# Kernel optimization log

Hardware: AMD Instinct MI355X
Metric: run time of the kernel (lower is better)

## Reference

```python
import jax, jax.numpy as jnp
import numpy as np

N_NODES = 100000
N_EDGES = 1600000
IN_C, HID_C, OUT_C = 64, 64, 16


def _sage_conv(x, src, dst, W_l, b_l, W_r, num_nodes):
    # PyG SAGEConv (aggr='mean'): out = lin_l(mean_{j->i} x_j) + lin_r(x_i)
    # aggregate first (cheap small-d features), then one GEMM
    msg_sum = jax.ops.segment_sum(x[src], dst, num_segments=num_nodes)
    deg = jax.ops.segment_sum(jnp.ones_like(dst, dtype=x.dtype), dst,
                              num_segments=num_nodes)
    mean = msg_sum / jnp.maximum(deg, 1.0)[:, None]
    return mean @ W_l + b_l + x @ W_r


def setup_inputs() -> dict:
    key = jax.random.key(0)
    ks = jax.random.split(key, 8)
    x = jax.random.normal(ks[0], (N_NODES, IN_C), dtype=jnp.float32)
    edge_index = jax.random.randint(ks[1], (2, N_EDGES), 0, N_NODES, dtype=jnp.int64)
    # Glorot-ish init for weights; lin_l has bias, lin_r has none (PyG default)
    def glorot(k, fan_in, fan_out):
        s = jnp.sqrt(6.0 / (fan_in + fan_out))
        return jax.random.uniform(k, (fan_in, fan_out), jnp.float32, -s, s)
    return {
        "x": x,
        "edge_index": edge_index,
        "W1_l": glorot(ks[2], IN_C, HID_C),
        "b1": jnp.zeros((HID_C,), jnp.float32),
        "W1_r": glorot(ks[3], IN_C, HID_C),
        "W2_l": glorot(ks[4], HID_C, OUT_C),
        "b2": jnp.zeros((OUT_C,), jnp.float32),
        "W2_r": glorot(ks[5], HID_C, OUT_C),
    }


def reference(x, edge_index, W1_l, b1, W1_r, W2_l, b2, W2_r):
    src, dst = edge_index[0], edge_index[1]
    h = _sage_conv(x, src, dst, W1_l, b1, W1_r, N_NODES)
    h = jax.nn.relu(h)
    # dropout p=0.3 is identity in eval mode
    out = _sage_conv(h, src, dst, W2_l, b2, W2_r, N_NODES)
    return out
```

## Files before the change

### kernel.cpp

```cpp
#include <hip/hip_runtime.h>
#include <hip/hip_fp16.h>

#define N_NODES 100000
#define N_EDGES 1600000
#define IN_C 64
#define HID_C 64
#define OUT_C 16

#define BKT 128
#define BSH 7
#define NBKT 782
#define CAP 2816
#define GSTR 32
#define GB 512
#define EPB 3125
#define NIT 13
#define G1B 1563

typedef _Float16 f16x8 __attribute__((ext_vector_type(8)));
typedef float f32x4 __attribute__((ext_vector_type(4)));
typedef float f32x16 __attribute__((ext_vector_type(16)));

__global__ __launch_bounds__(256) void k_merged1(
    const int* __restrict__ src, const int* __restrict__ dst,
    int* __restrict__ gcnt, int* __restrict__ binned,
    const float* __restrict__ x, const float* __restrict__ Wl,
    const float* __restrict__ Wr, const float* __restrict__ b,
    __half* __restrict__ p, __half* __restrict__ q) {
  __shared__ _Float16 sA[64 * 68];
  __shared__ _Float16 sW[128 * 68];
  int t = threadIdx.x;

  if (blockIdx.x < GB) {
    int* h   = (int*)sA;
    int* cur = (int*)sW;
    for (int i = t; i < NBKT; i += 256) h[i] = 0;
    __syncthreads();
    int base = blockIdx.x * EPB;
    int end = base + EPB;
    int dv[NIT], sv[NIT];
#pragma unroll
    for (int it = 0; it < NIT; ++it) {
      int e = base + t + it * 256;
      bool ok = (e < end);
      dv[it] = ok ? dst[e] : -1;
      sv[it] = ok ? src[e] : 0;
    }
#pragma unroll
    for (int it = 0; it < NIT; ++it)
      if (dv[it] >= 0) atomicAdd(&h[dv[it] >> BSH], 1);
    __syncthreads();
    for (int i = t; i < NBKT; i += 256) {
      int c = h[i];
      int b0 = (c > 0) ? atomicAdd(&gcnt[i * GSTR], c) : 0;
      cur[i] = i * CAP + b0;
    }
    __syncthreads();
#pragma unroll
    for (int it = 0; it < NIT; ++it) {
      if (dv[it] >= 0) {
        int d = dv[it];
        int pos = atomicAdd(&cur[d >> BSH], 1);
        binned[pos] = (sv[it] << BSH) | (d & (BKT - 1));
      }
    }
    return;
  }

  int n0 = (blockIdx.x - GB) * 64;

  for (int f = t; f < 1024; f += 256) {
    int r = f >> 4, c4 = f & 15;
    int n = n0 + r;
    float4 v = {0.0f, 0.0f, 0.0f, 0.0f};
    if (n < N_NODES) v = *(const float4*)&x[(size_t)n * 64 + c4 * 4];
    union { _Float16 h[4]; float2 f2; } u;
    u.h[0] = (_Float16)v.x; u.h[1] = (_Float16)v.y;
    u.h[2] = (_Float16)v.z; u.h[3] = (_Float16)v.w;
    *(float2*)&sA[r * 68 + c4 * 4] = u.f2;
  }
  for (int f = t; f < 2048; f += 256) {
    int k = f >> 5, c4 = f & 31;
    float4 w = (c4 < 16) ? *(const float4*)&Wl[k * 64 + c4 * 4]
                         : *(const float4*)&Wr[k * 64 + (c4 - 16) * 4];
    int c = c4 * 4;
    sW[(c + 0) * 68 + k] = (_Float16)w.x;
    sW[(c + 1) * 68 + k] = (_Float16)w.y;
    sW[(c + 2) * 68 + k] = (_Float16)w.z;
    sW[(c + 3) * 68 + k] = (_Float16)w.w;
  }
  __syncthreads();

  int w = t >> 6, lane = t & 63;
  int m = lane & 31, half = lane >> 5;
  int rt = w & 1, cg = w >> 1;

  f32x16 acc[2];
#pragma unroll
  for (int r = 0; r < 16; ++r) { acc[0][r] = 0.0f; acc[1][r] = 0.0f; }

  const _Float16* pA = &sA[(rt * 32 + m) * 68 + half * 8];
  const _Float16* pB0 = &sW[(cg * 64 + m) * 68 + half * 8];
  const _Float16* pB1 = &sW[(cg * 64 + 32 + m) * 68 + half * 8];
#pragma unroll
  for (int kc = 0; kc < 4; ++kc) {
    union { f16x8 v; float2 f2[2]; } a, b0, b1;
    a.f2[0] = *(const float2*)(pA + kc * 16);
    a.f2[1] = *(const float2*)(pA + kc * 16 + 4);
    b0.f2[0] = *(const float2*)(pB0 + kc * 16);
    b0.f2[1] = *(const float2*)(pB0 + kc * 16 + 4);
    b1.f2[0] = *(const float2*)(pB1 + kc * 16);
    b1.f2[1] = *(const float2*)(pB1 + kc * 16 + 4);
    acc[0] = __builtin_amdgcn_mfma_f32_32x32x16_f16(a.v, b0.v, acc[0], 0, 0, 0);
    acc[1] = __builtin_amdgcn_mfma_f32_32x32x16_f16(a.v, b1.v, acc[1], 0, 0, 0);
  }

  if (cg == 0) {
#pragma unroll
    for (int tt = 0; tt < 2; ++tt) {
      int col = tt * 32 + m;
#pragma unroll
      for (int r = 0; r < 16; ++r) {
        int row = (r & 3) + 4 * half + 8 * (r >> 2);
        int n = n0 + rt * 32 + row;
        if (n < N_NODES) p[(size_t)n * 64 + col] = __float2half(acc[tt][r]);
      }
    }
  } else {
    float bias[2] = {b[m], b[32 + m]};
#pragma unroll
    for (int tt = 0; tt < 2; ++tt) {
      int col = tt * 32 + m;
#pragma unroll
      for (int r = 0; r < 16; ++r) {
        int row = (r & 3) + 4 * half + 8 * (r >> 2);
        int n = n0 + rt * 32 + row;
        if (n < N_NODES)
          q[(size_t)n * 64 + col] = __float2half(acc[tt][r] + bias[tt]);
      }
    }
  }
}

__global__ __launch_bounds__(512) void k_fuse1c(
    const float4* __restrict__ p1, const int* __restrict__ gcnt,
    const int* __restrict__ binned, const float* __restrict__ W2l,
    const float* __restrict__ W2r, const float* __restrict__ b2,
    const float4* __restrict__ q1, int* __restrict__ csr,
    int* __restrict__ rowstart, int* __restrict__ cnt,
    __half* __restrict__ p2, float* __restrict__ q2) {
  __shared__ int hcnt[BKT];
  __shared__ int hscan[BKT];
  __shared__ int cur[BKT];
  __shared__ int lcsr[CAP];
  __shared__ _Float16 sH[BKT * 68];
  __shared__ _Float16 sW[32 * 68];
  int b = blockIdx.x;
  int t = threadIdx.x;

  {
    int k = t >> 3, c4v = t & 7;
    float4 w = (c4v < 4) ? *(const float4*)&W2l[k * 16 + c4v * 4]
                         : *(const float4*)&W2r[k * 16 + (c4v - 4) * 4];
    int c = c4v * 4;
    sW[(c + 0) * 68 + k] = (_Float16)w.x;
    sW[(c + 1) * 68 + k] = (_Float16)w.y;
    sW[(c + 2) * 68 + k] = (_Float16)w.z;
    sW[(c + 3) * 68 + k] = (_Float16)w.w;
  }
  if (t < BKT) hcnt[t] = 0;
  __syncthreads();

  int start = b * CAP;
  int total = gcnt[b * GSTR];
  for (int i = t; i < total; i += 512)
    atomicAdd(&hcnt[binned[start + i] & (BKT - 1)], 1);
  __syncthreads();
  if (t < 64) {
    int s0 = hcnt[t], s1 = hcnt[64 + t];
    for (int st = 1; st < 64; st <<= 1) {
      int a0 = __shfl_up(s0, st);
      int a1 = __shfl_up(s1, st);
      if (t >= st) { s0 += a0; s1 += a1; }
    }
    s1 += __shfl(s0, 63);
    hscan[t] = s0;
    hscan[64 + t] = s1;
  }
  __syncthreads();
  if (t < BKT) {
    int v = hcnt[t];
    int e0 = hscan[t] - v;
    cur[t] = e0;
    int n = (b << BSH) + t;
    if (n < N_NODES) {
      rowstart[n] = start + e0;
      cnt[n] = v;
    }
  }
  __syncthreads();
  for (int i = t; i < total; i += 512) {
    int vv = binned[start + i];
    int pos = atomicAdd(&cur[vv & (BKT - 1)], 1);
    lcsr[pos] = vv >> BSH;
  }
  __syncthreads();
  for (int i = t; i < total; i += 512) csr[start + i] = lcsr[i];

  int g = t >> 3, c4 = t & 7;
  for (int r = g; r < BKT; r += 64) {
    int n = (b << BSH) + r;
    if (n < N_NODES) {
      int deg = hcnt[r];
      int row = hscan[r] - deg;
      float acc[8];
#pragma unroll
      for (int m = 0; m < 8; ++m) acc[m] = 0.0f;
      int j = 0;
      for (; j + 8 <= deg; j += 8) {
        int idx[8];
#pragma unroll
        for (int u = 0; u < 8; ++u) idx[u] = lcsr[row + j + u];
        float4 av[8];
#pragma unroll
        for (int u = 0; u < 8; ++u) av[u] = p1[idx[u] * 8 + c4];
#pragma unroll
        for (int u = 0; u < 8; ++u) {
          const __half2* h = (const __half2*)&av[u];
#pragma unroll
          for (int m = 0; m < 4; ++m) {
            float2 f = __half22float2(h[m]);
            acc[2 * m] += f.x;
            acc[2 * m + 1] += f.y;
          }
        }
      }
      for (; j < deg; ++j) {
        float4 a = p1[lcsr[row + j] * 8 + c4];
        const __half2* h = (const __half2*)&a;
#pragma unroll
        for (int m = 0; m < 4; ++m) {
          float2 f = __half22float2(h[m]);
          acc[2 * m] += f.x;
          acc[2 * m + 1] += f.y;
        }
      }
      float inv = 1.0f / fmaxf((float)deg, 1.0f);
      float4 qv = q1[n * 8 + c4];
      __half2* qh = (__half2*)&qv;
      union { __half2 h2[2]; float2 f2; } u01, u23;
#pragma unroll
      for (int m = 0; m < 2; ++m) {
        float2 f = __half22float2(qh[m]);
        float2 s;
        s.x = fmaxf(acc[2 * m] * inv + f.x, 0.0f);
        s.y = fmaxf(acc[2 * m + 1] * inv + f.y, 0.0f);
        u01.h2[m] = __float22half2_rn(s);
      }
#pragma unroll
      for (int m = 2; m < 4; ++m) {
        float2 f = __half22float2(qh[m]);
        float2 s;
        s.x = fmaxf(acc[2 * m] * inv + f.x, 0.0f);
        s.y = fmaxf(acc[2 * m + 1] * inv + f.y, 0.0f);
        u23.h2[m - 2] = __float22half2_rn(s);
      }
      *(float2*)&sH[r * 68 + c4 * 8] = u01.f2;
      *(float2*)&sH[r * 68 + c4 * 8 + 4] = u23.f2;
    } else {
      *(float2*)&sH[r * 68 + c4 * 8] = make_float2(0.0f, 0.0f);
      *(float2*)&sH[r * 68 + c4 * 8 + 4] = make_float2(0.0f, 0.0f);
    }
  }
  __syncthreads();

  int wv = t >> 6, lane = t & 63;
  int n16 = lane & 15, quad = lane >> 4;
  f32x4 aP, aQ;
#pragma unroll
  for (int r = 0; r < 4; ++r) { aP[r] = 0.0f; aQ[r] = 0.0f; }
  const _Float16* pA = &sH[(wv * 16 + n16) * 68 + quad * 8];
  const _Float16* pBP = &sW[n16 * 68 + quad * 8];
  const _Float16* pBQ = &sW[(16 + n16) * 68 + quad * 8];
#pragma unroll
  for (int kc = 0; kc < 2; ++kc) {
    union { f16x8 v; float2 f2[2]; } a, bp, bq;
    a.f2[0] = *(const float2*)(pA + kc * 32);
    a.f2[1] = *(const float2*)(pA + kc * 32 + 4);
    bp.f2[0] = *(const float2*)(pBP + kc * 32);
    bp.f2[1] = *(const float2*)(pBP + kc * 32 + 4);
    bq.f2[0] = *(const float2*)(pBQ + kc * 32);
    bq.f2[1] = *(const float2*)(pBQ + kc * 32 + 4);
    aP = __builtin_amdgcn_mfma_f32_16x16x32_f16(a.v, bp.v, aP, 0, 0, 0);
    aQ = __builtin_amdgcn_mfma_f32_16x16x32_f16(a.v, bq.v, aQ, 0, 0, 0);
  }
  float bias = b2[n16];
#pragma unroll
  for (int r = 0; r < 4; ++r) {
    int row = wv * 16 + quad * 4 + r;
    int n = (b << BSH) + row;
    if (n < N_NODES) {
      p2[(size_t)n * 16 + n16] = __float2half(aP[r]);
      q2[(size_t)n * 16 + n16] = aQ[r] + bias;
    }
  }
}

__global__ __launch_bounds__(256) void k_fuse2(
    const float4* __restrict__ p2, const float4* __restrict__ q2,
    const int* __restrict__ rowstart, const int* __restrict__ cnt,
    const int* __restrict__ csr, float4* __restrict__ out) {
  int t = threadIdx.x;
  int n = blockIdx.x * 128 + (t >> 1);
  if (n >= N_NODES) return;
  int c8 = t & 1;
  int row = rowstart[n];
  int deg = cnt[n];
  float acc[8];
#pragma unroll
  for (int m = 0; m < 8; ++m) acc[m] = 0.0f;
  int j = 0;
  for (; j + 8 <= deg; j += 8) {
    int idx[8];
#pragma unroll
    for (int u = 0; u < 8; ++u) idx[u] = csr[row + j + u];
    float4 av[8];
#pragma unroll
    for (int u = 0; u < 8; ++u) av[u] = p2[idx[u] * 2 + c8];
#pragma unroll
    for (int u = 0; u < 8; ++u) {
      const __half2* h = (const __half2*)&av[u];
#pragma unroll
      for (int m = 0; m < 4; ++m) {
        float2 f = __half22float2(h[m]);
        acc[2 * m] += f.x;
        acc[2 * m + 1] += f.y;
      }
    }
  }
  for (; j < deg; ++j) {
    float4 a = p2[csr[row + j] * 2 + c8];
    const __half2* h = (const __half2*)&a;
#pragma unroll
    for (int m = 0; m < 4; ++m) {
      float2 f = __half22float2(h[m]);
      acc[2 * m] += f.x;
      acc[2 * m + 1] += f.y;
    }
  }
  float inv = 1.0f / fmaxf((float)deg, 1.0f);
  float4 q0 = q2[n * 4 + c8 * 2];
  float4 q1v = q2[n * 4 + c8 * 2 + 1];
  float4 o0 = {acc[0] * inv + q0.x, acc[1] * inv + q0.y,
               acc[2] * inv + q0.z, acc[3] * inv + q0.w};
  float4 o1 = {acc[4] * inv + q1v.x, acc[5] * inv + q1v.y,
               acc[6] * inv + q1v.z, acc[7] * inv + q1v.w};
  out[n * 4 + c8 * 2] = o0;
  out[n * 4 + c8 * 2 + 1] = o1;
}

extern "C" void kernel_launch(void* const* d_in, const int* in_sizes, int n_in,
                              void* d_out, int out_size, void* d_ws, size_t ws_size,
                              hipStream_t stream) {
  const float* x   = (const float*)d_in[0];
  const int* edge  = (const int*)d_in[1];
  const int* src   = edge;
  const int* dst   = edge + N_EDGES;
  const float* W1l = (const float*)d_in[2];
  const float* b1  = (const float*)d_in[3];
  const float* W1r = (const float*)d_in[4];
  const float* W2l = (const float*)d_in[5];
  const float* b2  = (const float*)d_in[6];
  const float* W2r = (const float*)d_in[7];
  float* out = (float*)d_out;

  int* gcnt     = (int*)d_ws;
  int* rowstart = gcnt + 25088;
  int* cnt      = rowstart + N_NODES;
  int* binned   = cnt + N_NODES;
  int* csr      = binned + NBKT * CAP;
  __half* p1    = (__half*)(csr + NBKT * CAP);
  __half* q1    = p1 + (size_t)N_NODES * 64;
  __half* p2    = q1 + (size_t)N_NODES * 64;
  float* q2     = (float*)(p2 + (size_t)N_NODES * 16);

  hipMemsetAsync(gcnt, 0, NBKT * GSTR * sizeof(int), stream);

  k_merged1<<<GB + G1B, 256, 0, stream>>>(src, dst, gcnt, binned,
                                          x, W1l, W1r, b1, p1, q1);
  k_fuse1c<<<NBKT, 512, 0, stream>>>((const float4*)p1, gcnt, binned,
                                     W2l, W2r, b2, (const float4*)q1,
                                     csr, rowstart, cnt, p2, q2);
  k_fuse2<<<(N_NODES + 127) / 128, 256, 0, stream>>>((const float4*)p2,
                                                     (const float4*)q2,
                                                     rowstart, cnt, csr,
                                                     (float4*)out);
}
```

Before: 191.5 us.

## Fuse layer-2 aggregation into bucket kernel via grid barrier, double bucket size

Merges the final aggregation kernel into the CSR/layer-1 kernel. A software grid-wide barrier (an atomic counter plus spin) waits until every block has written p2, then each block gathers layer-2 features using its CSR kept in LDS. It also keeps q2 in LDS, and stops writing the global csr, rowstart, cnt and q2 arrays. Bucket size grows from 128 to 256 nodes, giving 391 blocks of 512 threads, and edges are held in registers instead of being re-read from global. This removes one launch and several global round trips. The cost is a grid barrier that deadlocks unless all blocks are co-resident, and much larger LDS use per block.

```diff
diff --git a/kernel.cpp b/kernel.cpp
--- a/kernel.cpp
+++ b/kernel.cpp
@@ -7,10 +7,10 @@
 #define HID_C 64
 #define OUT_C 16
 
-#define BKT 128
-#define BSH 7
-#define NBKT 782
-#define CAP 2816
+#define BKT 256
+#define BSH 8
+#define NBKT 391
+#define CAP 5120
 #define GSTR 32
 #define GB 512
 #define EPB 3125
@@ -93,15 +93,15 @@
 
   int w = t >> 6, lane = t & 63;
   int m = lane & 31, half = lane >> 5;
-  int rt = w & 1, cg = w >> 1;
+  int rt = w & 1, cg2 = w >> 1;
 
   f32x16 acc[2];
 #pragma unroll
   for (int r = 0; r < 16; ++r) { acc[0][r] = 0.0f; acc[1][r] = 0.0f; }
 
   const _Float16* pA = &sA[(rt * 32 + m) * 68 + half * 8];
-  const _Float16* pB0 = &sW[(cg * 64 + m) * 68 + half * 8];
-  const _Float16* pB1 = &sW[(cg * 64 + 32 + m) * 68 + half * 8];
+  const _Float16* pB0 = &sW[(cg2 * 64 + m) * 68 + half * 8];
+  const _Float16* pB1 = &sW[(cg2 * 64 + 32 + m) * 68 + half * 8];
 #pragma unroll
   for (int kc = 0; kc < 4; ++kc) {
     union { f16x8 v; float2 f2[2]; } a, b0, b1;
@@ -115,7 +115,7 @@
     acc[1] = __builtin_amdgcn_mfma_f32_32x32x16_f16(a.v, b1.v, acc[1], 0, 0, 0);
   }
 
-  if (cg == 0) {
+  if (cg2 == 0) {
 #pragma unroll
     for (int tt = 0; tt < 2; ++tt) {
       int col = tt * 32 + m;
@@ -142,18 +142,17 @@
   }
 }
 
-__global__ __launch_bounds__(512) void k_fuse1c(
+__global__ __launch_bounds__(512, 4) void k_fuse12(
     const float4* __restrict__ p1, const int* __restrict__ gcnt,
     const int* __restrict__ binned, const float* __restrict__ W2l,
     const float* __restrict__ W2r, const float* __restrict__ b2,
-    const float4* __restrict__ q1, int* __restrict__ csr,
-    int* __restrict__ rowstart, int* __restrict__ cnt,
-    __half* __restrict__ p2, float* __restrict__ q2) {
+    const float4* __restrict__ q1, __half* __restrict__ p2,
+    int* __restrict__ bar, float4* __restrict__ out) {
   __shared__ int hcnt[BKT];
   __shared__ int hscan[BKT];
   __shared__ int cur[BKT];
   __shared__ int lcsr[CAP];
-  __shared__ _Float16 sH[BKT * 68];
+  __shared__ _Float16 sH[256 * 68];
   __shared__ _Float16 sW[32 * 68];
   int b = blockIdx.x;
   int t = threadIdx.x;
@@ -173,39 +172,41 @@
 
   int start = b * CAP;
   int total = gcnt[b * GSTR];
-  for (int i = t; i < total; i += 512)
-    atomicAdd(&hcnt[binned[start + i] & (BKT - 1)], 1);
+  int ev[10];
+#pragma unroll
+  for (int u = 0; u < 10; ++u) {
+    int i = t + u * 512;
+    ev[u] = (i < total) ? binned[start + i] : -1;
+  }
+#pragma unroll
+  for (int u = 0; u < 10; ++u)
+    if (ev[u] >= 0) atomicAdd(&hcnt[ev[u] & (BKT - 1)], 1);
   __syncthreads();
   if (t < 64) {
-    int s0 = hcnt[t], s1 = hcnt[64 + t];
+    int s0 = hcnt[t], s1 = hcnt[64 + t], s2 = hcnt[128 + t], s3 = hcnt[192 + t];
     for (int st = 1; st < 64; st <<= 1) {
-      int a0 = __shfl_up(s0, st);
-      int a1 = __shfl_up(s1, st);
-      if (t >= st) { s0 += a0; s1 += a1; }
-    }
-    s1 += __shfl(s0, 63);
+      int a0 = __shfl_up(s0, st), a1 = __shfl_up(s1, st);
+      int a2 = __shfl_up(s2, st), a3 = __shfl_up(s3, st);
+      if (t >= st) { s0 += a0; s1 += a1; s2 += a2; s3 += a3; }
+    }
+    int t0 = __shfl(s0, 63), t1 = __shfl(s1, 63), t2 = __shfl(s2, 63);
     hscan[t] = s0;
-    hscan[64 + t] = s1;
-  }
-  __syncthreads();
-  if (t < BKT) {
-    int v = hcnt[t];
-    int e0 = hscan[t] - v;
-    cur[t] = e0;
-    int n = (b << BSH) + t;
-    if (n < N_NODES) {
-      rowstart[n] = start + e0;
-      cnt[n] = v;
-    }
-  }
-  __syncthreads();
-  for (int i = t; i < total; i += 512) {
-    int vv = binned[start + i];
-    int pos = atomicAdd(&cur[vv & (BKT - 1)], 1);
-    lcsr[pos] = vv >> BSH;
-  }
-  __syncthreads();
-  for (int i = t; i < total; i += 512) csr[start + i] = lcsr[i];
+    hscan[64 + t] = s1 + t0;
+    hscan[128 + t] = s2 + t0 + t1;
+    hscan[192 + t] = s3 + t0 + t1 + t2;
+  }
+  __syncthreads();
+  if (t < BKT) cur[t] = hscan[t] - hcnt[t];
+  __syncthreads();
+#pragma unroll
+  for (int u = 0; u < 10; ++u) {
+    if (ev[u] >= 0) {
+      int vv = ev[u];
+      int pos = atomicAdd(&cur[vv & (BKT - 1)], 1);
+      lcsr[pos] = vv >> BSH;
+    }
+  }
+  __syncthreads();
 
   int g = t >> 3, c4 = t & 7;
   for (int r = g; r < BKT; r += 64) {
@@ -276,87 +277,111 @@
 
   int wv = t >> 6, lane = t & 63;
   int n16 = lane & 15, quad = lane >> 4;
-  f32x4 aP, aQ;
-#pragma unroll
-  for (int r = 0; r < 4; ++r) { aP[r] = 0.0f; aQ[r] = 0.0f; }
-  const _Float16* pA = &sH[(wv * 16 + n16) * 68 + quad * 8];
-  const _Float16* pBP = &sW[n16 * 68 + quad * 8];
-  const _Float16* pBQ = &sW[(16 + n16) * 68 + quad * 8];
-#pragma unroll
-  for (int kc = 0; kc < 2; ++kc) {
-    union { f16x8 v; float2 f2[2]; } a, bp, bq;
-    a.f2[0] = *(const float2*)(pA + kc * 32);
-    a.f2[1] = *(const float2*)(pA + kc * 32 + 4);
-    bp.f2[0] = *(const float2*)(pBP + kc * 32);
-    bp.f2[1] = *(const float2*)(pBP + kc * 32 + 4);
-    bq.f2[0] = *(const float2*)(pBQ + kc * 32);
-    bq.f2[1] = *(const float2*)(pBQ + kc * 32 + 4);
-    aP = __builtin_amdgcn_mfma_f32_16x16x32_f16(a.v, bp.v, aP, 0, 0, 0);
-    aQ = __builtin_amdgcn_mfma_f32_16x16x32_f16(a.v, bq.v, aQ, 0, 0, 0);
-  }
   float bias = b2[n16];
-#pragma unroll
-  for (int r = 0; r < 4; ++r) {
-    int row = wv * 16 + quad * 4 + r;
-    int n = (b << BSH) + row;
+  float q2v[2][4];
+#pragma unroll
+  for (int h2 = 0; h2 < 2; ++h2) {
+    int tile = wv + h2 * 8;
+    f32x4 aP, aQ;
+#pragma unroll
+    for (int r = 0; r < 4; ++r) { aP[r] = 0.0f; aQ[r] = 0.0f; }
+    const _Float16* pA = &sH[(tile * 16 + n16) * 68 + quad * 8];
+    const _Float16* pBP = &sW[n16 * 68 + quad * 8];
+    const _Float16* pBQ = &sW[(16 + n16) * 68 + quad * 8];
+#pragma unroll
+    for (int kc = 0; kc < 2; ++kc) {
+      union { f16x8 v; float2 f2[2]; } a, bp, bq;
+      a.f2[0] = *(const float2*)(pA + kc * 32);
+      a.f2[1] = *(const float2*)(pA + kc * 32 + 4);
+      bp.f2[0] = *(const float2*)(pBP + kc * 32);
+      bp.f2[1] = *(const float2*)(pBP + kc * 32 + 4);
+      bq.f2[0] = *(const float2*)(pBQ + kc * 32);
+      bq.f2[1] = *(const float2*)(pBQ + kc * 32 + 4);
+      aP = __builtin_amdgcn_mfma_f32_16x16x32_f16(a.v, bp.v, aP, 0, 0, 0);
+      aQ = __builtin_amdgcn_mfma_f32_16x16x32_f16(a.v, bq.v, aQ, 0, 0, 0);
+    }
+#pragma unroll
+    for (int r = 0; r < 4; ++r) {
+      int row = tile * 16 + quad * 4 + r;
+      int n = (b << BSH) + row;
+      if (n < N_NODES) p2[(size_t)n * 16 + n16] = __float2half(aP[r]);
+      q2v[h2][r] = aQ[r] + bias;
+    }
+  }
+  __syncthreads();
+  float* q2l = (float*)sH;
+#pragma unroll
+  for (int h2 = 0; h2 < 2; ++h2) {
+#pragma unroll
+    for (int r = 0; r < 4; ++r) {
+      int row = (wv + h2 * 8) * 16 + quad * 4 + r;
+      q2l[row * 16 + n16] = q2v[h2][r];
+    }
+  }
+
+  __syncthreads();
+  if (t == 0) {
+    __threadfence();
+    atomicAdd(bar, 1);
+    int spins = 0;
+    while (__hip_atomic_load(bar, __ATOMIC_RELAXED,
+                             __HIP_MEMORY_SCOPE_AGENT) < NBKT) {
+      __builtin_amdgcn_s_sleep(2);
+      if (++spins > 10000000) break;
+    }
+    __threadfence();
+  }
+  __syncthreads();
+
+  {
+    int r = t >> 1, c8 = t & 1;
+    int n = (b << BSH) + r;
     if (n < N_NODES) {
-      p2[(size_t)n * 16 + n16] = __float2half(aP[r]);
-      q2[(size_t)n * 16 + n16] = aQ[r] + bias;
-    }
-  }
-}
-
-__global__ __launch_bounds__(256) void k_fuse2(
-    const float4* __restrict__ p2, const float4* __restrict__ q2,
-    const int* __restrict__ rowstart, const int* __restrict__ cnt,
-    const int* __restrict__ csr, float4* __restrict__ out) {
-  int t = threadIdx.x;
-  int n = blockIdx.x * 128 + (t >> 1);
-  if (n >= N_NODES) return;
-  int c8 = t & 1;
-  int row = rowstart[n];
-  int deg = cnt[n];
-  float acc[8];
-#pragma unroll
-  for (int m = 0; m < 8; ++m) acc[m] = 0.0f;
-  int j = 0;
-  for (; j + 8 <= deg; j += 8) {
-    int idx[8];
-#pragma unroll
-    for (int u = 0; u < 8; ++u) idx[u] = csr[row + j + u];
-    float4 av[8];
-#pragma unroll
-    for (int u = 0; u < 8; ++u) av[u] = p2[idx[u] * 2 + c8];
-#pragma unroll
-    for (int u = 0; u < 8; ++u) {
-      const __half2* h = (const __half2*)&av[u];
-#pragma unroll
-      for (int m = 0; m < 4; ++m) {
-        float2 f = __half22float2(h[m]);
-        acc[2 * m] += f.x;
-        acc[2 * m + 1] += f.y;
-      }
-    }
-  }
-  for (; j < deg; ++j) {
-    float4 a = p2[csr[row + j] * 2 + c8];
-    const __half2* h = (const __half2*)&a;
-#pragma unroll
-    for (int m = 0; m < 4; ++m) {
-      float2 f = __half22float2(h[m]);
-      acc[2 * m] += f.x;
-      acc[2 * m + 1] += f.y;
-    }
-  }
-  float inv = 1.0f / fmaxf((float)deg, 1.0f);
-  float4 q0 = q2[n * 4 + c8 * 2];
-  float4 q1v = q2[n * 4 + c8 * 2 + 1];
-  float4 o0 = {acc[0] * inv + q0.x, acc[1] * inv + q0.y,
-               acc[2] * inv + q0.z, acc[3] * inv + q0.w};
-  float4 o1 = {acc[4] * inv + q1v.x, acc[5] * inv + q1v.y,
-               acc[6] * inv + q1v.z, acc[7] * inv + q1v.w};
-  out[n * 4 + c8 * 2] = o0;
-  out[n * 4 + c8 * 2 + 1] = o1;
+      int deg = hcnt[r];
+      int row0 = hscan[r] - deg;
+      float acc[8];
+#pragma unroll
+      for (int m = 0; m < 8; ++m) acc[m] = 0.0f;
+      const float4* p2v = (const float4*)p2;
+      int j = 0;
+      for (; j + 8 <= deg; j += 8) {
+        int idx[8];
+#pragma unroll
+        for (int u = 0; u < 8; ++u) idx[u] = lcsr[row0 + j + u];
+        float4 av[8];
+#pragma unroll
+        for (int u = 0; u < 8; ++u) av[u] = p2v[idx[u] * 2 + c8];
+#pragma unroll
+        for (int u = 0; u < 8; ++u) {
+          const __half2* h = (const __half2*)&av[u];
+#pragma unroll
+          for (int m = 0; m < 4; ++m) {
+            float2 f = __half22float2(h[m]);
+            acc[2 * m] += f.x;
+            acc[2 * m + 1] += f.y;
+          }
+        }
+      }
+      for (; j < deg; ++j) {
+        float4 a = p2v[lcsr[row0 + j] * 2 + c8];
+        const __half2* h = (const __half2*)&a;
+#pragma unroll
+        for (int m = 0; m < 4; ++m) {
+          float2 f = __half22float2(h[m]);
+          acc[2 * m] += f.x;
+          acc[2 * m + 1] += f.y;
+        }
+      }
+      float inv = 1.0f / fmaxf((float)deg, 1.0f);
+      const float* qr = &q2l[r * 16 + c8 * 8];
+      float4 o0 = {acc[0] * inv + qr[0], acc[1] * inv + qr[1],
+                   acc[2] * inv + qr[2], acc[3] * inv + qr[3]};
+      float4 o1 = {acc[4] * inv + qr[4], acc[5] * inv + qr[5],
+                   acc[6] * inv + qr[6], acc[7] * inv + qr[7]};
+      out[n * 4 + c8 * 2] = o0;
+      out[n * 4 + c8 * 2 + 1] = o1;
+    }
+  }
 }
 
 extern "C" void kernel_launch(void* const* d_in, const int* in_sizes, int n_in,
@@ -375,24 +400,17 @@
   float* out = (float*)d_out;
 
   int* gcnt     = (int*)d_ws;
-  int* rowstart = gcnt + 25088;
-  int* cnt      = rowstart + N_NODES;
-  int* binned   = cnt + N_NODES;
-  int* csr      = binned + NBKT * CAP;
-  __half* p1    = (__half*)(csr + NBKT * CAP);
+  int* bar      = gcnt + 12512;
+  int* binned   = gcnt + 12544;
+  __half* p1    = (__half*)(binned + NBKT * CAP);
   __half* q1    = p1 + (size_t)N_NODES * 64;
   __half* p2    = q1 + (size_t)N_NODES * 64;
-  float* q2     = (float*)(p2 + (size_t)N_NODES * 16);
-
-  hipMemsetAsync(gcnt, 0, NBKT * GSTR * sizeof(int), stream);
+
+  hipMemsetAsync(gcnt, 0, 12544 * sizeof(int), stream);
 
   k_merged1<<<GB + G1B, 256, 0, stream>>>(src, dst, gcnt, binned,
                                           x, W1l, W1r, b1, p1, q1);
-  k_fuse1c<<<NBKT, 512, 0, stream>>>((const float4*)p1, gcnt, binned,
+  k_fuse12<<<NBKT, 512, 0, stream>>>((const float4*)p1, gcnt, binned,
                                      W2l, W2r, b2, (const float4*)q1,
-                                     csr, rowstart, cnt, p2, q2);
-  k_fuse2<<<(N_NODES + 127) / 128, 256, 0, stream>>>((const float4*)p2,
-                                                     (const float4*)q2,
-                                                     rowstart, cnt, csr,
-                                                     (float4*)out);
+                                     p2, bar, (float4*)out);
 }
```

Result: slower. 215.6 us (+12.6%).

## Double node bucket size, replicate binning histograms, and register-cache bucket edges

Applied to the files above, without the earlier changes.

Node buckets grow from 128 to 256 nodes, halving the number of buckets, and the per-bucket fused kernel now runs with 1024 threads and a four-segment scan. The edge-binning histogram is replicated four ways in shared memory to reduce LDS atomic contention. Bucket edges are loaded once into registers and reused for both the count and scatter passes instead of being read twice from global memory. The risks are fewer, larger blocks, so less parallelism across the GPU, and much higher LDS use per block, which may reduce occupancy.

```diff
diff --git a/kernel.cpp b/kernel.cpp
--- a/kernel.cpp
+++ b/kernel.cpp
@@ -7,10 +7,10 @@
 #define HID_C 64
 #define OUT_C 16
 
-#define BKT 128
-#define BSH 7
-#define NBKT 782
-#define CAP 2816
+#define BKT 256
+#define BSH 8
+#define NBKT 391
+#define CAP 5120
 #define GSTR 32
 #define GB 512
 #define EPB 3125
@@ -32,9 +32,9 @@
   int t = threadIdx.x;
 
   if (blockIdx.x < GB) {
-    int* h   = (int*)sA;
+    int* h4  = (int*)sA;
     int* cur = (int*)sW;
-    for (int i = t; i < NBKT; i += 256) h[i] = 0;
+    for (int i = t; i < 4 * NBKT; i += 256) h4[i] = 0;
     __syncthreads();
     int base = blockIdx.x * EPB;
     int end = base + EPB;
@@ -46,12 +46,13 @@
       dv[it] = ok ? dst[e] : -1;
       sv[it] = ok ? src[e] : 0;
     }
+    int hoff = (t & 3) * NBKT;
 #pragma unroll
     for (int it = 0; it < NIT; ++it)
-      if (dv[it] >= 0) atomicAdd(&h[dv[it] >> BSH], 1);
+      if (dv[it] >= 0) atomicAdd(&h4[hoff + (dv[it] >> BSH)], 1);
     __syncthreads();
     for (int i = t; i < NBKT; i += 256) {
-      int c = h[i];
+      int c = h4[i] + h4[NBKT + i] + h4[2 * NBKT + i] + h4[3 * NBKT + i];
       int b0 = (c > 0) ? atomicAdd(&gcnt[i * GSTR], c) : 0;
       cur[i] = i * CAP + b0;
     }
@@ -142,7 +143,7 @@
   }
 }
 
-__global__ __launch_bounds__(512) void k_fuse1c(
+__global__ __launch_bounds__(1024) void k_fuse1c(
     const float4* __restrict__ p1, const int* __restrict__ gcnt,
     const int* __restrict__ binned, const float* __restrict__ W2l,
     const float* __restrict__ W2r, const float* __restrict__ b2,
@@ -153,12 +154,12 @@
   __shared__ int hscan[BKT];
   __shared__ int cur[BKT];
   __shared__ int lcsr[CAP];
-  __shared__ _Float16 sH[BKT * 68];
+  __shared__ _Float16 sH[256 * 68];
   __shared__ _Float16 sW[32 * 68];
   int b = blockIdx.x;
   int t = threadIdx.x;
 
-  {
+  if (t < 512) {
     int k = t >> 3, c4v = t & 7;
     float4 w = (c4v < 4) ? *(const float4*)&W2l[k * 16 + c4v * 4]
                          : *(const float4*)&W2r[k * 16 + (c4v - 4) * 4];
@@ -173,19 +174,28 @@
 
   int start = b * CAP;
   int total = gcnt[b * GSTR];
-  for (int i = t; i < total; i += 512)
-    atomicAdd(&hcnt[binned[start + i] & (BKT - 1)], 1);
+  int ev[5];
+#pragma unroll
+  for (int u = 0; u < 5; ++u) {
+    int i = t + u * 1024;
+    ev[u] = (i < total) ? binned[start + i] : -1;
+  }
+#pragma unroll
+  for (int u = 0; u < 5; ++u)
+    if (ev[u] >= 0) atomicAdd(&hcnt[ev[u] & (BKT - 1)], 1);
   __syncthreads();
   if (t < 64) {
-    int s0 = hcnt[t], s1 = hcnt[64 + t];
+    int s0 = hcnt[t], s1 = hcnt[64 + t], s2 = hcnt[128 + t], s3 = hcnt[192 + t];
     for (int st = 1; st < 64; st <<= 1) {
-      int a0 = __shfl_up(s0, st);
-      int a1 = __shfl_up(s1, st);
-      if (t >= st) { s0 += a0; s1 += a1; }
-    }
-    s1 += __shfl(s0, 63);
+      int a0 = __shfl_up(s0, st), a1 = __shfl_up(s1, st);
+      int a2 = __shfl_up(s2, st), a3 = __shfl_up(s3, st);
+      if (t >= st) { s0 += a0; s1 += a1; s2 += a2; s3 += a3; }
+    }
+    int t0 = __shfl(s0, 63), t1 = __shfl(s1, 63), t2 = __shfl(s2, 63);
     hscan[t] = s0;
-    hscan[64 + t] = s1;
+    hscan[64 + t] = s1 + t0;
+    hscan[128 + t] = s2 + t0 + t1;
+    hscan[192 + t] = s3 + t0 + t1 + t2;
   }
   __syncthreads();
   if (t < BKT) {
@@ -199,16 +209,19 @@
     }
   }
   __syncthreads();
-  for (int i = t; i < total; i += 512) {
-    int vv = binned[start + i];
-    int pos = atomicAdd(&cur[vv & (BKT - 1)], 1);
-    lcsr[pos] = vv >> BSH;
-  }
-  __syncthreads();
-  for (int i = t; i < total; i += 512) csr[start + i] = lcsr[i];
+#pragma unroll
+  for (int u = 0; u < 5; ++u) {
+    if (ev[u] >= 0) {
+      int vv = ev[u];
+      int pos = atomicAdd(&cur[vv & (BKT - 1)], 1);
+      lcsr[pos] = vv >> BSH;
+    }
+  }
+  __syncthreads();
+  for (int i = t; i < total; i += 1024) csr[start + i] = lcsr[i];
 
   int g = t >> 3, c4 = t & 7;
-  for (int r = g; r < BKT; r += 64) {
+  for (int r = g; r < BKT; r += 128) {
     int n = (b << BSH) + r;
     if (n < N_NODES) {
       int deg = hcnt[r];
@@ -375,7 +388,7 @@
   float* out = (float*)d_out;
 
   int* gcnt     = (int*)d_ws;
-  int* rowstart = gcnt + 25088;
+  int* rowstart = gcnt + 12544;
   int* cnt      = rowstart + N_NODES;
   int* binned   = cnt + N_NODES;
   int* csr      = binned + NBKT * CAP;
@@ -388,9 +401,9 @@
 
   k_merged1<<<GB + G1B, 256, 0, stream>>>(src, dst, gcnt, binned,
                                           x, W1l, W1r, b1, p1, q1);
-  k_fuse1c<<<NBKT, 512, 0, stream>>>((const float4*)p1, gcnt, binned,
-                                     W2l, W2r, b2, (const float4*)q1,
-                                     csr, rowstart, cnt, p2, q2);
+  k_fuse1c<<<NBKT, 1024, 0, stream>>>((const float4*)p1, gcnt, binned,
+                                      W2l, W2r, b2, (const float4*)q1,
+                                      csr, rowstart, cnt, p2, q2);
   k_fuse2<<<(N_NODES + 127) / 128, 256, 0, stream>>>((const float4*)p2,
                                                      (const float4*)q2,
                                                      rowstart, cnt, csr,
```

After: 184.2 us. -3.8%, faster.
